# Optimization experiments

Measured on AMD Instinct MI355X. Metric: run time of the kernel, lower is better.

The kernel has to match this reference:

```python
import jax, jax.numpy as jnp
import numpy as np

B, N, C, H, D, M = 8, 4096, 512, 8, 64, 16
TOPK = 3
TAU = 0.1
DIV_REG = 0.01


def setup_inputs() -> dict:
    key = jax.random.key(0)
    ks = jax.random.split(key, 12)
    w = lambda i, shape: 0.02 * jax.random.normal(ks[i], shape, dtype=jnp.float32)
    return {
        "x": jax.random.normal(ks[0], (B, N, C), dtype=jnp.float32),
        "W_qkv": w(1, (C, 3 * C)),                    # qkv_bias=False
        "W_proj": w(2, (C, C)), "b_proj": jnp.zeros((C,), jnp.float32),
        "W_rspec": w(3, (C, H * M)), "b_rspec": jnp.zeros((H * M,), jnp.float32),
        "W_rspat": w(4, (C, H * M)), "b_rspat": jnp.zeros((H * M,), jnp.float32),
        "K_spec": w(5, (H, M, D)),                    # prototype banks (EMA buffers)
        "K_spat": w(6, (H, M, D)),
        "W_tok": w(7, (D, D)), "b_tok": jnp.zeros((D,), jnp.float32),
        "W_prot": w(8, (D, D)), "b_prot": jnp.zeros((D,), jnp.float32),
    }


def topk_mask_from_logits(logits, k):
    # keep top-k of softmax probs along last axis, renormalize
    vals = jax.lax.top_k(logits, k)[0]
    thresh = vals[..., -1:]
    mask = (logits >= thresh).astype(logits.dtype)
    probs = jax.nn.softmax(logits, axis=-1) * mask
    denom = jnp.maximum(jnp.sum(probs, axis=-1, keepdims=True), 1e-6)
    return probs / denom


def _l2norm(a, eps):
    return a / jnp.maximum(jnp.linalg.norm(a, axis=-1, keepdims=True), eps)


def reference(x, W_qkv, W_proj, b_proj, W_rspec, b_rspec, W_rspat, b_rspat,
              K_spec, K_spat, W_tok, b_tok, W_prot, b_prot):
    # qkv: [B,N,3C] -> q,k,v each [B,H,N,D]
    qkv = (x @ W_qkv).reshape(B, N, 3, H, D).transpose(2, 0, 3, 1, 4)
    q, _k, v = qkv[0], qkv[1], qkv[2]

    # routing logits [B,H,N,M] -> top-k masked probs
    r_spec = topk_mask_from_logits(
        (x @ W_rspec + b_rspec).reshape(B, N, H, M).transpose(0, 2, 1, 3), TOPK)
    r_spat = topk_mask_from_logits(
        (x @ W_rspat + b_rspat).reshape(B, N, H, M).transpose(0, 2, 1, 3), TOPK)

    # effective keys from prototype banks: [B,H,N,D]
    K_eff = (jnp.einsum('bhnm,hmd->bhnd', r_spec, K_spec)
             + jnp.einsum('bhnm,hmd->bhnd', r_spat, K_spat))
    K_norm = jax.nn.softmax(K_eff, axis=-2)          # softmax over tokens N

    # linear attention reorder: context [B,H,D,D], then Q @ context
    context = jnp.einsum('bhnd,bhne->bhde', K_norm, v)
    out = jnp.einsum('bhnd,bhde->bhne', q, context)  # note: scale unused in source
    out = out.transpose(0, 2, 1, 3).reshape(B, N, C) @ W_proj + b_proj

    # ---- contrastive aux loss ----
    t_n = _l2norm(v @ W_tok + b_tok, 1e-12)          # [B,H,N,D]
    p_spec_n = _l2norm(K_spec @ W_prot + b_prot, 1e-12)
    p_spat_n = _l2norm(K_spat @ W_prot + b_prot, 1e-12)
    sim_spec = jnp.einsum('bhnd,hmd->bhnm', t_n, p_spec_n)
    sim_spat = jnp.einsum('bhnd,hmd->bhnm', t_n, p_spat_n)
    pos_spec = jnp.sum(sim_spec * r_spec, axis=-1)
    pos_spat = jnp.sum(sim_spat * r_spat, axis=-1)
    loss_spec = -jnp.mean(pos_spec / TAU - jax.nn.logsumexp(sim_spec / TAU, axis=-1))
    loss_spat = -jnp.mean(pos_spat / TAU - jax.nn.logsumexp(sim_spat / TAU, axis=-1))
    contrastive_loss = 0.5 * (loss_spec + loss_spat)

    def diversity_loss(P):
        h, m, _d = P.shape
        p = P / jnp.maximum(jnp.linalg.norm(P, axis=-1, keepdims=True), 1e-6)
        sim = jnp.einsum('hmd,hnd->hmn', p, p)
        mask = 1.0 - jnp.eye(m, dtype=P.dtype)[None]
        return jnp.sum(sim * mask) / (h * m * (m - 1) + 1e-6)

    diversity = DIV_REG * (diversity_loss(K_spec) + diversity_loss(K_spat))
    return out, contrastive_loss, diversity
```

## Files before the change

kernel.cpp:

```cpp
#include <hip/hip_runtime.h>
#include <math.h>

#define B_ 8
#define N_ 4096
#define C_ 512
#define H_ 8
#define D_ 64
#define M_ 16
#define BN_TOK (B_*N_)
#define TAU_ 0.1f

typedef short s8v __attribute__((ext_vector_type(8)));
typedef float f4v __attribute__((ext_vector_type(4)));
typedef unsigned short u16;

__device__ __forceinline__ float wave_reduce_sum(float v){
  #pragma unroll
  for (int o = 32; o > 0; o >>= 1) v += __shfl_xor(v, o);
  return v;
}

__device__ __forceinline__ unsigned short f2b(float f){
  unsigned int u = __float_as_uint(f);
  u += 0x7fffu + ((u >> 16) & 1u);
  return (unsigned short)(u >> 16);
}

__device__ __forceinline__ float b2f(u16 b){
  return __uint_as_float(((unsigned int)b) << 16);
}

__device__ __forceinline__ s8v pack8(const float* f){
  s8v r;
  #pragma unroll
  for (int e = 0; e < 8; ++e) r[e] = (short)f2b(f[e]);
  return r;
}

__device__ __forceinline__ void gload16(const u16* g, u16* l){
  __builtin_amdgcn_global_load_lds(
      (const __attribute__((address_space(1))) unsigned int*)g,
      (__attribute__((address_space(3))) unsigned int*)l, 16, 0, 0);
}

__global__ __launch_bounds__(256) void prep_all(const float* __restrict__ x, u16* __restrict__ xb,
                                                const float* __restrict__ W_qkv,
                                                const float* __restrict__ W_rspec,
                                                const float* __restrict__ W_rspat,
                                                const float* __restrict__ W_proj,
                                                u16* __restrict__ Wt_qv,
                                                u16* __restrict__ Wt_r,
                                                u16* __restrict__ Wt_p){
  const int bid = blockIdx.x;
  if (bid < 1024) {
    const int n8 = (BN_TOK*C_)/8;
    for (int i = bid * 256 + threadIdx.x; i < n8; i += 1024*256) {
      const float4* p = (const float4*)(x + (size_t)i * 8);
      float4 a = p[0], b = p[1];
      float f[8] = {a.x,a.y,a.z,a.w,b.x,b.y,b.z,b.w};
      *(s8v*)(xb + (size_t)i * 8) = pack8(f);
    }
    return;
  }
  const int r = bid - 1024, k = threadIdx.x;
  const float* src; int ld, coff, n; u16* dst;
  if (r < 512)       { src = W_qkv;   ld = 1536; coff = 0;    n = r;        dst = Wt_qv; }
  else if (r < 1024) { src = W_qkv;   ld = 1536; coff = 1024; n = r - 512;  dst = Wt_qv + 512*512; }
  else if (r < 1152) { src = W_rspec; ld = 128;  coff = 0;    n = r - 1024; dst = Wt_r; }
  else if (r < 1280) { src = W_rspat; ld = 128;  coff = 0;    n = r - 1152; dst = Wt_r + 128*512; }
  else               { src = W_proj;  ld = 512;  coff = 0;    n = r - 1280; dst = Wt_p; }
  dst[(size_t)n*512 + k]       = f2b(src[(size_t)k*ld + coff + n]);
  dst[(size_t)n*512 + k + 256] = f2b(src[(size_t)(k+256)*ld + coff + n]);
}

template<bool OUT_BF16>
__global__ __launch_bounds__(256) void gemm_bt(const u16* __restrict__ A,
                                               const u16* __restrict__ Bt,
                                               const float* __restrict__ bias,
                                               void* __restrict__ C,
                                               int K, int lda, int ldc, int bt_bstride) {
  __shared__ __align__(16) u16 Asm[2][2][128*32];
  __shared__ __align__(16) u16 Bsm[2][2][128*32];
  const int tid = threadIdx.x;
  const int lane = tid & 63, w = tid >> 6;
  const int bm = blockIdx.x * 128, bn = blockIdx.y * 128;

  const int lrow = lane >> 2;
  const int kch  = ((lane & 3) ^ ((lane >> 3) & 3)) << 3;

  const u16* Btb = Bt + (size_t)(bm >> 12) * bt_bstride;
  const u16* Ag0 = A   + (size_t)(bm + w*16 + lrow) * lda + kch;
  const u16* Ag1 = Ag0 + (size_t)64 * lda;
  const u16* Bg0 = Btb + (size_t)(bn + w*16 + lrow) * K + kch;
  const u16* Bg1 = Bg0 + (size_t)64 * K;
  const int l0 = (w*16)*32, l1 = (w*16+64)*32;

  const int lm = lane & 15, lg = lane >> 4;
  const int w0 = (w >> 1) * 64, c0 = (w & 1) * 64;
  const int xs = (lg ^ ((lm >> 1) & 3)) << 3;

  const int NSTEP = K >> 6;

  f4v acc[4][4];
  #pragma unroll
  for (int i = 0; i < 4; ++i)
    #pragma unroll
    for (int j = 0; j < 4; ++j) acc[i][j] = (f4v){0.f,0.f,0.f,0.f};

  #define STAGE(buf, t)                                         \
    gload16(Ag0 + (t)*64,      &Asm[buf][0][l0]);               \
    gload16(Ag1 + (t)*64,      &Asm[buf][0][l1]);               \
    gload16(Ag0 + (t)*64 + 32, &Asm[buf][1][l0]);               \
    gload16(Ag1 + (t)*64 + 32, &Asm[buf][1][l1]);               \
    gload16(Bg0 + (t)*64,      &Bsm[buf][0][l0]);               \
    gload16(Bg1 + (t)*64,      &Bsm[buf][0][l1]);               \
    gload16(Bg0 + (t)*64 + 32, &Bsm[buf][1][l0]);               \
    gload16(Bg1 + (t)*64 + 32, &Bsm[buf][1][l1]);

  STAGE(0, 0)
  STAGE(1, 1)

  int cur = 0;
  for (int k = 0; k < NSTEP; ++k) {
    if (k < NSTEP - 1) asm volatile("s_waitcnt vmcnt(8)" ::: "memory");
    else               asm volatile("s_waitcnt vmcnt(0)" ::: "memory");
    __builtin_amdgcn_s_barrier();
    __builtin_amdgcn_sched_barrier(0);

    #pragma unroll
    for (int h = 0; h < 2; ++h) {
      s8v af[4], bf_[4];
      #pragma unroll
      for (int i = 0; i < 4; ++i) af[i]  = *(const s8v*)&Asm[cur][h][(w0 + 16*i + lm)*32 + xs];
      #pragma unroll
      for (int j = 0; j < 4; ++j) bf_[j] = *(const s8v*)&Bsm[cur][h][(c0 + 16*j + lm)*32 + xs];
      #pragma unroll
      for (int i = 0; i < 4; ++i)
        #pragma unroll
        for (int j = 0; j < 4; ++j)
          acc[i][j] = __builtin_amdgcn_mfma_f32_16x16x32_bf16(af[i], bf_[j], acc[i][j], 0, 0, 0);
    }

    __builtin_amdgcn_sched_barrier(0);
    __builtin_amdgcn_s_barrier();
    if (k + 2 < NSTEP) {
      STAGE(cur, k + 2)
    }
    __builtin_amdgcn_sched_barrier(0);
    cur ^= 1;
  }
  #undef STAGE

  #pragma unroll
  for (int j = 0; j < 4; ++j) {
    const int col = bn + c0 + 16*j + lm;
    const float bj = (!OUT_BF16 && bias) ? bias[col] : 0.f;
    #pragma unroll
    for (int i = 0; i < 4; ++i) {
      const int row = bm + w0 + 16*i + 4*lg;
      #pragma unroll
      for (int r = 0; r < 4; ++r) {
        if (OUT_BF16) ((u16*)C)[(size_t)(row + r) * ldc + col] = f2b(acc[i][j][r]);
        else          ((float*)C)[(size_t)(row + r) * ldc + col] = acc[i][j][r] + bj;
      }
    }
  }
}

__global__ __launch_bounds__(256) void router_topk(const float* __restrict__ logits,
                            const float* __restrict__ b_rspec, const float* __restrict__ b_rspat,
                            float* __restrict__ r_spec, float* __restrict__ r_spat,
                            u16* __restrict__ rb_spec, u16* __restrict__ rb_spat) {
  int t = blockIdx.x * blockDim.x + threadIdx.x;
  if (t >= BN_TOK * H_ * 2) return;
  int route = t & 1, h = (t >> 1) & 7, bn = t >> 4;
  int b = bn >> 12, n = bn & 4095;
  const float* lg = logits + (size_t)bn*256 + route*128 + h*16;
  const float* bias = (route ? b_rspat : b_rspec) + h*16;
  float v[16];
  #pragma unroll
  for (int m=0;m<16;++m) v[m] = lg[m] + bias[m];
  float m1=-1e30f, m2=-1e30f, m3=-1e30f;
  #pragma unroll
  for (int m=0;m<16;++m){
    float x=v[m];
    if (x>m1){m3=m2;m2=m1;m1=x;}
    else if (x>m2){m3=m2;m2=x;}
    else if (x>m3){m3=x;}
  }
  float S=0.f, Sm=0.f, e[16];
  #pragma unroll
  for (int m=0;m<16;++m){ e[m]=expf(v[m]-m1); S+=e[m]; if (v[m]>=m3) Sm+=e[m]; }
  float denom = fmaxf(Sm/S, 1e-6f);
  float inv = 1.f/(S*denom);
  size_t idx = (((size_t)b*H_ + h)*N_ + n)*16;
  float* r = (route ? r_spat : r_spec) + idx;
  u16* rb  = (route ? rb_spat : rb_spec) + idx;
  #pragma unroll
  for (int m=0;m<16;++m) {
    float val = (v[m] >= m3) ? e[m]*inv : 0.f;
    r[m] = val;
    rb[m] = f2b(val);
  }
}

__global__ __launch_bounds__(256) void context_mfma(const u16* __restrict__ rb_spec, const u16* __restrict__ rb_spat,
                               const float* __restrict__ K_spec, const float* __restrict__ K_spat,
                               const u16* __restrict__ qvb, float* __restrict__ pctx, float* __restrict__ pZ) {
  const int chunk = blockIdx.x & 15, bh = blockIdx.x >> 4;
  const int b = bh >> 3, h = bh & 7;
  const int tid = threadIdx.x;
  const int lane = tid & 63, w = tid >> 6;
  const int lm = lane & 15, lg = lane >> 4;

  __shared__ __align__(16) unsigned short Kc[64*32];
  __shared__ __align__(16) unsigned short Rs[64*32];
  __shared__ __align__(16) unsigned short Vt[64*64];
  __shared__ __align__(16) unsigned short Ps[64*64];
  __shared__ float Zs[256];

  {
    int d = tid & 63, c = tid >> 6;
    float f[8];
    #pragma unroll
    for (int u = 0; u < 8; ++u) {
      int k = c*8 + u;
      f[u] = (k < 16) ? K_spec[h*1024 + k*64 + d] : K_spat[h*1024 + (k-16)*64 + d];
    }
    *(s8v*)&Kc[d*32 + ((c ^ (d&3)) << 3)] = pack8(f);
  }

  const u16* rsg = rb_spec + ((size_t)bh*N_ + chunk*256)*16;
  const u16* rtg = rb_spat + ((size_t)bh*N_ + chunk*256)*16;
  const u16* vbase = qvb + 512 + h*64;
  const size_t tokbase = (size_t)b*N_ + chunk*256;

  f4v acc2[4];
  #pragma unroll
  for (int j = 0; j < 4; ++j) acc2[j] = (f4v){0.f,0.f,0.f,0.f};
  float zreg[4] = {0.f,0.f,0.f,0.f};

  for (int t0 = 0; t0 < 4; ++t0) {
    __syncthreads();
    {
      int n = tid & 63, c = tid >> 6;
      const u16* src = (c < 2 ? rsg : rtg) + ((size_t)(t0*64 + n))*16 + (c&1)*8;
      *(s8v*)&Rs[n*32 + ((c ^ (n&3)) << 3)] = *(const s8v*)src;
    }
    {
      int n = tid & 63, eq = tid >> 6;
      const u16* src = vbase + (tokbase + t0*64 + n)*1024 + eq*16;
      u16 f[16];
      *(s8v*)&f[0] = ((const s8v*)src)[0];
      *(s8v*)&f[8] = ((const s8v*)src)[1];
      #pragma unroll
      for (int u = 0; u < 16; ++u) {
        int e = eq*16 + u;
        Vt[e*64 + ((((n>>3) ^ (e&7)) << 3) | (n&7))] = f[u];
      }
    }
    __syncthreads();
    {
      s8v a1 = *(const s8v*)&Rs[(16*w + lm)*32 + ((lg ^ (lm&3)) << 3)];
      #pragma unroll
      for (int j = 0; j < 4; ++j) {
        s8v b1 = *(const s8v*)&Kc[(16*j + lm)*32 + ((lg ^ (lm&3)) << 3)];
        f4v c1 = (f4v){0.f,0.f,0.f,0.f};
        c1 = __builtin_amdgcn_mfma_f32_16x16x32_bf16(a1, b1, c1, 0, 0, 0);
        float p0 = expf(c1[0]), p1 = expf(c1[1]), p2 = expf(c1[2]), p3 = expf(c1[3]);
        float zz = p0 + p1 + p2 + p3;
        zz += __shfl_xor(zz, 16); zz += __shfl_xor(zz, 32);
        zreg[j] += zz;
        int d = 16*j + lm;
        int n0w = 16*w + 4*lg;
        Ps[d*64 + (((((n0w  )>>3) ^ (d&7)) << 3) | ((n0w  )&7))] = f2b(p0);
        Ps[d*64 + (((((n0w+1)>>3) ^ (d&7)) << 3) | ((n0w+1)&7))] = f2b(p1);
        Ps[d*64 + (((((n0w+2)>>3) ^ (d&7)) << 3) | ((n0w+2)&7))] = f2b(p2);
        Ps[d*64 + (((((n0w+3)>>3) ^ (d&7)) << 3) | ((n0w+3)&7))] = f2b(p3);
      }
    }
    __syncthreads();
    #pragma unroll
    for (int kb = 0; kb < 2; ++kb) {
      s8v a2 = *(const s8v*)&Vt[(16*w + lm)*64 + (((kb*4 + lg) ^ (lm&7)) << 3)];
      #pragma unroll
      for (int j = 0; j < 4; ++j) {
        s8v b2 = *(const s8v*)&Ps[(16*j + lm)*64 + (((kb*4 + lg) ^ (lm&7)) << 3)];
        acc2[j] = __builtin_amdgcn_mfma_f32_16x16x32_bf16(a2, b2, acc2[j], 0, 0, 0);
      }
    }
  }
  float* pc = pctx + (size_t)(bh*16 + chunk)*4096;
  #pragma unroll
  for (int j = 0; j < 4; ++j) {
    #pragma unroll
    for (int r = 0; r < 4; ++r)
      pc[(16*w + 4*lg + r)*64 + 16*j + lm] = acc2[j][r];
    if (lg == 0) Zs[w*64 + 16*j + lm] = zreg[j];
  }
  __syncthreads();
  if (tid < 64)
    pZ[(size_t)(bh*16 + chunk)*64 + tid] = Zs[tid] + Zs[64+tid] + Zs[128+tid] + Zs[192+tid];
}

__global__ __launch_bounds__(256) void context_reduce(const float* __restrict__ pctx, const float* __restrict__ pZ,
                              float* __restrict__ ctx) {
  const int gid = blockIdx.x * 256 + threadIdx.x;
  const int bh = gid >> 12, e = (gid >> 6) & 63, d = gid & 63;
  float z = 0.f, s = 0.f;
  for (int c = 0; c < 16; ++c) {
    z += pZ[(size_t)(bh*16 + c)*64 + d];
    s += pctx[(size_t)(bh*16 + c)*4096 + e*64 + d];
  }
  ctx[(size_t)bh*4096 + e*64 + d] = s / z;
}

__global__ __launch_bounds__(256) void cwt_kernel(const float* __restrict__ ctx, const u16* __restrict__ Wt_p,
                                                  u16* __restrict__ CWt) {
  const int bh = blockIdx.x >> 3, oct = blockIdx.x & 7;
  const int b = bh >> 3, h = bh & 7;
  const int tid = threadIdx.x;
  __shared__ float ctxS[64*64];
  __shared__ u16 WsL[64*64];
  {
    int e = tid >> 2, dq = tid & 3;
    const float4* src = (const float4*)(ctx + (size_t)bh*4096 + e*64 + dq*16);
    float4* dst = (float4*)(ctxS + e*64 + dq*16);
    dst[0] = src[0]; dst[1] = src[1]; dst[2] = src[2]; dst[3] = src[3];
  }
  const int c0 = oct * 64;
  {
    int cl = tid >> 2, eq = tid & 3;
    const s8v* src = (const s8v*)(Wt_p + (size_t)(c0 + cl)*512 + h*64 + eq*16);
    *(s8v*)&WsL[cl*64 + eq*16]     = src[0];
    *(s8v*)&WsL[cl*64 + eq*16 + 8] = src[1];
  }
  __syncthreads();
  const int d = tid & 63, cq = tid >> 6;
  for (int ci = 0; ci < 16; ++ci) {
    int cl = cq*16 + ci;
    float acc = 0.f;
    #pragma unroll
    for (int e = 0; e < 64; ++e)
      acc = fmaf(ctxS[e*64 + d], b2f(WsL[cl*64 + e]), acc);
    CWt[((size_t)b*512 + (c0 + cl))*512 + h*64 + d] = f2b(acc);
  }
}

__global__ __launch_bounds__(64) void protnorm_div(const float* __restrict__ K_spec, const float* __restrict__ K_spat,
                               const float* __restrict__ W_prot, const float* __restrict__ b_prot,
                               float* __restrict__ pnorm, float* __restrict__ pdiv) {
  const int bid = blockIdx.x;
  const int e = threadIdx.x;
  if (bid < 256) {
    int route = bid >> 7, hm = bid & 127;
    const float* Km = (route ? K_spat : K_spec) + hm*64;
    __shared__ float kv[64];
    kv[e] = Km[e];
    __syncthreads();
    float acc = b_prot[e];
    for (int dcol = 0; dcol < 64; ++dcol) acc = fmaf(kv[dcol], W_prot[dcol*64 + e], acc);
    float n2 = wave_reduce_sum(acc*acc);
    pnorm[(size_t)bid*64 + e] = acc / fmaxf(sqrtf(n2), 1e-12f);
    return;
  }
  const int db = bid - 256;
  int route = db >> 3, h = db & 7;
  const float* Km = (route ? K_spat : K_spec) + h*16*64;
  float s = 0.f, selfsum = 0.f;
  for (int m = 0; m < 16; ++m) {
    float x = Km[m*64 + e];
    float n2 = wave_reduce_sum(x*x);
    float p = x / fmaxf(sqrtf(n2), 1e-6f);
    s += p; selfsum += p*p;
  }
  float off = wave_reduce_sum(s*s - selfsum);
  if (e == 0) pdiv[db] = off;
}

__global__ __launch_bounds__(256) void contrastive_mfma(const u16* __restrict__ qvb,
                                   const float* __restrict__ r_spec, const float* __restrict__ r_spat,
                                   const float* __restrict__ W_tok, const float* __restrict__ b_tok,
                                   const float* __restrict__ pnorm, float* __restrict__ pcontr) {
  const int tile = blockIdx.x & 255;
  const int h = blockIdx.x >> 8;
  const int t0 = tile * 128;
  const int b = t0 >> 12;
  const int n0 = t0 & 4095;
  const int tid = threadIdx.x;
  const int lane = tid & 63, w = tid >> 6;
  const int lm = lane & 15, lg = lane >> 4;

  __shared__ __align__(16) unsigned short Usm[128*72];
  __shared__ __align__(16) unsigned short Wsm[64*72];
  __shared__ __align__(16) unsigned short Psm[32*72];
  __shared__ float nrmS[128];
  __shared__ float btkS[64];
  __shared__ float bred[2][4];
  float* Uf = (float*)Usm;

  {
    const int vr = tid >> 1, vh = tid & 1;
    const u16* vg = qvb + (size_t)(b*N_ + n0 + vr)*1024 + 512 + h*64 + vh*32;
    #pragma unroll
    for (int c = 0; c < 4; ++c) *(s8v*)&Usm[vr*72 + vh*32 + c*8] = ((const s8v*)vg)[c];
  }
  {
    const int e = tid & 63, kh = tid >> 6;
    float f[16];
    #pragma unroll
    for (int rr = 0; rr < 16; ++rr) f[rr] = W_tok[(size_t)(kh*16+rr)*64 + e];
    *(s8v*)&Wsm[e*72 + kh*16]     = pack8(&f[0]);
    *(s8v*)&Wsm[e*72 + kh*16 + 8] = pack8(&f[8]);
  }
  if (tid < 128) {
    const int proto = tid >> 2, q4 = tid & 3;
    const int src = (proto < 16) ? (h*16 + proto) : (128 + h*16 + (proto-16));
    const float* pg = pnorm + (size_t)src*64 + q4*16;
    float f[16];
    #pragma unroll
    for (int i = 0; i < 4; ++i) {
      float4 v4 = ((const float4*)pg)[i];
      f[4*i]=v4.x; f[4*i+1]=v4.y; f[4*i+2]=v4.z; f[4*i+3]=v4.w;
    }
    *(s8v*)&Psm[proto*72 + q4*16]     = pack8(&f[0]);
    *(s8v*)&Psm[proto*72 + q4*16 + 8] = pack8(&f[8]);
  }
  if (tid < 64) btkS[tid] = b_tok[tid];
  __syncthreads();

  f4v acc[2][4];
  #pragma unroll
  for (int i=0;i<2;++i)
    #pragma unroll
    for (int j=0;j<4;++j) acc[i][j] = (f4v){0.f,0.f,0.f,0.f};
  {
    s8v bf0[4], bf1[4];
    #pragma unroll
    for (int j=0;j<4;++j) {
      bf0[j] = *(const s8v*)&Wsm[(j*16+lm)*72 + lg*8];
      bf1[j] = *(const s8v*)&Wsm[(j*16+lm)*72 + 32 + lg*8];
    }
    #pragma unroll
    for (int i=0;i<2;++i) {
      s8v af0 = *(const s8v*)&Usm[(w*32+16*i+lm)*72 + lg*8];
      s8v af1 = *(const s8v*)&Usm[(w*32+16*i+lm)*72 + 32 + lg*8];
      #pragma unroll
      for (int j=0;j<4;++j) {
        acc[i][j] = __builtin_amdgcn_mfma_f32_16x16x32_bf16(af0, bf0[j], acc[i][j], 0, 0, 0);
        acc[i][j] = __builtin_amdgcn_mfma_f32_16x16x32_bf16(af1, bf1[j], acc[i][j], 0, 0, 0);
      }
    }
  }
  #pragma unroll
  for (int i=0;i<2;++i) {
    #pragma unroll
    for (int r=0;r<4;++r) {
      float s = 0.f;
      #pragma unroll
      for (int j=0;j<4;++j) {
        float val = acc[i][j][r] + btkS[j*16+lm];
        acc[i][j][r] = val;
        s += val*val;
      }
      s += __shfl_xor(s,1); s += __shfl_xor(s,2); s += __shfl_xor(s,4); s += __shfl_xor(s,8);
      if (lm == 0) nrmS[w*32 + 16*i + lg*4 + r] = s;
    }
  }
  #pragma unroll
  for (int i=0;i<2;++i)
    #pragma unroll
    for (int j=0;j<4;++j)
      #pragma unroll
      for (int r=0;r<4;++r)
        Usm[(w*32+16*i+lg*4+r)*72 + j*16+lm] = f2b(acc[i][j][r]);
  __syncthreads();

  f4v acc2[2][2];
  #pragma unroll
  for (int i=0;i<2;++i)
    #pragma unroll
    for (int j=0;j<2;++j) acc2[i][j] = (f4v){0.f,0.f,0.f,0.f};
  {
    s8v bf0[2], bf1[2];
    #pragma unroll
    for (int j=0;j<2;++j) {
      bf0[j] = *(const s8v*)&Psm[(j*16+lm)*72 + lg*8];
      bf1[j] = *(const s8v*)&Psm[(j*16+lm)*72 + 32 + lg*8];
    }
    #pragma unroll
    for (int i=0;i<2;++i) {
      s8v af0 = *(const s8v*)&Usm[(w*32+16*i+lm)*72 + lg*8];
      s8v af1 = *(const s8v*)&Usm[(w*32+16*i+lm)*72 + 32 + lg*8];
      #pragma unroll
      for (int j=0;j<2;++j) {
        acc2[i][j] = __builtin_amdgcn_mfma_f32_16x16x32_bf16(af0, bf0[j], acc2[i][j], 0, 0, 0);
        acc2[i][j] = __builtin_amdgcn_mfma_f32_16x16x32_bf16(af1, bf1[j], acc2[i][j], 0, 0, 0);
      }
    }
  }
  #pragma unroll
  for (int i=0;i<2;++i)
    #pragma unroll
    for (int j=0;j<2;++j)
      #pragma unroll
      for (int r=0;r<4;++r)
        Uf[(w*32+16*i+lg*4+r)*36 + j*16+lm] = acc2[i][j][r];
  __syncthreads();

  float l = 0.f;
  {
    const int tt = tid >> 1, route = tid & 1;
    float inv = 1.f / fmaxf(sqrtf(nrmS[tt]), 1e-12f);
    const float* rg = (route ? r_spat : r_spec) + (((size_t)b*H_ + h)*N_ + n0 + tt)*16;
    float s0[16];
    #pragma unroll
    for (int m=0;m<16;++m) s0[m] = Uf[tt*36 + route*16 + m]*inv;
    float pos = 0.f, mx = -1e30f;
    #pragma unroll
    for (int m=0;m<16;++m) {
      pos += s0[m]*rg[m];
      mx = fmaxf(mx, s0[m]);
    }
    float z = 0.f;
    #pragma unroll
    for (int m=0;m<16;++m) z += expf((s0[m]-mx)/TAU_);
    l = pos/TAU_ - (mx/TAU_ + logf(z));
  }
  float lspec = (tid & 1) ? 0.f : l;
  float lspat = (tid & 1) ? l : 0.f;
  lspec = wave_reduce_sum(lspec);
  lspat = wave_reduce_sum(lspat);
  if (lane == 0) { bred[0][w]=lspec; bred[1][w]=lspat; }
  __syncthreads();
  if (tid == 0) {
    pcontr[2*blockIdx.x]     = bred[0][0]+bred[0][1]+bred[0][2]+bred[0][3];
    pcontr[2*blockIdx.x + 1] = bred[1][0]+bred[1][1]+bred[1][2]+bred[1][3];
  }
}

__global__ __launch_bounds__(256) void finalize_kernel(const float* __restrict__ pcontr,
                                                       const float* __restrict__ pdiv,
                                                       float* __restrict__ tail) {
  __shared__ float red[2][4];
  const int tid = threadIdx.x, lane = tid & 63, w = tid >> 6;
  float ls = 0.f, lt = 0.f;
  for (int k = tid; k < 2048; k += 256) { ls += pcontr[2*k]; lt += pcontr[2*k + 1]; }
  ls = wave_reduce_sum(ls);
  lt = wave_reduce_sum(lt);
  if (lane == 0) { red[0][w] = ls; red[1][w] = lt; }
  __syncthreads();
  if (tid == 0) {
    float sspec = red[0][0]+red[0][1]+red[0][2]+red[0][3];
    float sspat = red[1][0]+red[1][1]+red[1][2]+red[1][3];
    float dspec = 0.f, dspat = 0.f;
    for (int k = 0; k < 8; ++k) { dspec += pdiv[k]; dspat += pdiv[8+k]; }
    float loss_spec = -(sspec / (float)(B_*H_*N_));
    float loss_spat = -(sspat / (float)(B_*H_*N_));
    float denom = (float)(H_*M_*(M_-1)) + 1e-6f;
    tail[0] = 0.5f*(loss_spec + loss_spat);
    tail[1] = 0.01f * (dspec/denom + dspat/denom);
  }
}

extern "C" void kernel_launch(void* const* d_in, const int* in_sizes, int n_in,
                              void* d_out, int out_size, void* d_ws, size_t ws_size,
                              hipStream_t stream) {
  const float* x       = (const float*)d_in[0];
  const float* W_qkv   = (const float*)d_in[1];
  const float* W_proj  = (const float*)d_in[2];
  const float* b_proj  = (const float*)d_in[3];
  const float* W_rspec = (const float*)d_in[4];
  const float* b_rspec = (const float*)d_in[5];
  const float* W_rspat = (const float*)d_in[6];
  const float* b_rspat = (const float*)d_in[7];
  const float* K_spec  = (const float*)d_in[8];
  const float* K_spat  = (const float*)d_in[9];
  const float* W_tok   = (const float*)d_in[10];
  const float* b_tok   = (const float*)d_in[11];
  const float* W_prot  = (const float*)d_in[12];
  const float* b_prot  = (const float*)d_in[13];
  float* out = (float*)d_out;

  float* ws = (float*)d_ws;
  u16*   qvb     = (u16*)ws;
  float* logits  = ws + 16777216;
  float* pctx    = ws + 16777216;
  float* pZ      = ws + 16777216 + 4194304;
  float* r_spec  = ws + 25165824;
  float* r_spat  = ws + 29360128;
  u16*   rb_spec = (u16*)(ws + 33554432);
  u16*   rb_spat = (u16*)(ws + 35651584);
  u16*   xb      = (u16*)(ws + 37748736);
  u16*   Wt_qv   = (u16*)(ws + 46137344);
  u16*   Wt_r    = (u16*)(ws + 46399488);
  u16*   Wt_p    = (u16*)(ws + 46465024);
  float* ctxb    = ws + 46596096;
  float* pnorm   = ws + 46858240;
  float* pcontr  = ws + 46874624;
  float* pdiv    = ws + 46878720;
  u16*   CWt     = (u16*)(ws + 46878736);

  dim3 blk256(256);

  prep_all<<<2816, blk256, 0, stream>>>(x, xb, W_qkv, W_rspec, W_rspat, W_proj, Wt_qv, Wt_r, Wt_p);

  gemm_bt<false><<<dim3(256,2), blk256, 0, stream>>>(xb, Wt_r, nullptr, logits, 512, 512, 256, 0);
  router_topk<<<2048, blk256, 0, stream>>>(logits, b_rspec, b_rspat, r_spec, r_spat, rb_spec, rb_spat);
  gemm_bt<true><<<dim3(256,8), blk256, 0, stream>>>(xb, Wt_qv, nullptr, qvb, 512, 512, 1024, 0);
  context_mfma<<<1024, blk256, 0, stream>>>(rb_spec, rb_spat, K_spec, K_spat, qvb, pctx, pZ);
  context_reduce<<<1024, blk256, 0, stream>>>(pctx, pZ, ctxb);
  cwt_kernel<<<512, blk256, 0, stream>>>(ctxb, Wt_p, CWt);
  protnorm_div<<<272, dim3(64), 0, stream>>>(K_spec, K_spat, W_prot, b_prot, pnorm, pdiv);
  contrastive_mfma<<<2048, blk256, 0, stream>>>(qvb, r_spec, r_spat, W_tok, b_tok, pnorm, pcontr);
  gemm_bt<false><<<dim3(256,4), blk256, 0, stream>>>(qvb, CWt, b_proj, out, 512, 1024, 512, 512*512);
  finalize_kernel<<<1, blk256, 0, stream>>>(pcontr, pdiv, out + 16777216);
}
```

Baseline: 334.1 us.

## Fuse router and QV GEMMs into one launch with XCD-aware tile mapping

Runs the routing-logit GEMM and the Q/V projection GEMM as a single launch over the contiguous concatenated transposed weights. Column tiles below the split are written as bf16 to qvb, and the rest go as fp32 to logits. Block IDs are also remapped so that each XCD owns a contiguous range of row tiles, which keeps shared A tiles in that XCD's L2. The aim is to cut one launch, fill the GPU better, and improve cache reuse. The cost is extra template and epilogue branching, and the fusion relies on Wt_r sitting directly after Wt_qv in the workspace.

```diff
diff --git a/kernel.cpp b/kernel.cpp
--- a/kernel.cpp
+++ b/kernel.cpp
@@ -73,17 +73,24 @@
   dst[(size_t)n*512 + k + 256] = f2b(src[(size_t)(k+256)*ld + coff + n]);
 }
 
-template<bool OUT_BF16>
+template<int MODE>
 __global__ __launch_bounds__(256) void gemm_bt(const u16* __restrict__ A,
                                                const u16* __restrict__ Bt,
                                                const float* __restrict__ bias,
                                                void* __restrict__ C,
-                                               int K, int lda, int ldc, int bt_bstride) {
+                                               float* __restrict__ C2,
+                                               int K, int lda, int ldc, int ldc2,
+                                               int split, int bt_bstride, int nm) {
   __shared__ __align__(16) u16 Asm[2][2][128*32];
   __shared__ __align__(16) u16 Bsm[2][2][128*32];
   const int tid = threadIdx.x;
   const int lane = tid & 63, w = tid >> 6;
-  const int bm = blockIdx.x * 128, bn = blockIdx.y * 128;
+
+  const int bid = blockIdx.x;
+  const int xcd = bid & 7, j = bid >> 3;
+  const int nmx = nm >> 3;
+  const int bm = (xcd * nmx + (j % nmx)) * 128;
+  const int bn = (j / nmx) * 128;
 
   const int lrow = lane >> 2;
   const int kch  = ((lane & 3) ^ ((lane >> 3) & 3)) << 3;
@@ -105,7 +112,7 @@
   #pragma unroll
   for (int i = 0; i < 4; ++i)
     #pragma unroll
-    for (int j = 0; j < 4; ++j) acc[i][j] = (f4v){0.f,0.f,0.f,0.f};
+    for (int j2 = 0; j2 < 4; ++j2) acc[i][j2] = (f4v){0.f,0.f,0.f,0.f};
 
   #define STAGE(buf, t)                                         \
     gload16(Ag0 + (t)*64,      &Asm[buf][0][l0]);               \
@@ -133,12 +140,12 @@
       #pragma unroll
       for (int i = 0; i < 4; ++i) af[i]  = *(const s8v*)&Asm[cur][h][(w0 + 16*i + lm)*32 + xs];
       #pragma unroll
-      for (int j = 0; j < 4; ++j) bf_[j] = *(const s8v*)&Bsm[cur][h][(c0 + 16*j + lm)*32 + xs];
+      for (int j2 = 0; j2 < 4; ++j2) bf_[j2] = *(const s8v*)&Bsm[cur][h][(c0 + 16*j2 + lm)*32 + xs];
       #pragma unroll
       for (int i = 0; i < 4; ++i)
         #pragma unroll
-        for (int j = 0; j < 4; ++j)
-          acc[i][j] = __builtin_amdgcn_mfma_f32_16x16x32_bf16(af[i], bf_[j], acc[i][j], 0, 0, 0);
+        for (int j2 = 0; j2 < 4; ++j2)
+          acc[i][j2] = __builtin_amdgcn_mfma_f32_16x16x32_bf16(af[i], bf_[j2], acc[i][j2], 0, 0, 0);
     }
 
     __builtin_amdgcn_sched_barrier(0);
@@ -151,17 +158,19 @@
   }
   #undef STAGE
 
-  #pragma unroll
-  for (int j = 0; j < 4; ++j) {
-    const int col = bn + c0 + 16*j + lm;
-    const float bj = (!OUT_BF16 && bias) ? bias[col] : 0.f;
+  const bool tobf = (MODE == 1) || (MODE == 2 && bn < split);
+  #pragma unroll
+  for (int j2 = 0; j2 < 4; ++j2) {
+    const int col = bn + c0 + 16*j2 + lm;
+    const float bj = (MODE == 0 && bias) ? bias[col] : 0.f;
     #pragma unroll
     for (int i = 0; i < 4; ++i) {
       const int row = bm + w0 + 16*i + 4*lg;
       #pragma unroll
       for (int r = 0; r < 4; ++r) {
-        if (OUT_BF16) ((u16*)C)[(size_t)(row + r) * ldc + col] = f2b(acc[i][j][r]);
-        else          ((float*)C)[(size_t)(row + r) * ldc + col] = acc[i][j][r] + bj;
+        if (tobf)            ((u16*)C)[(size_t)(row + r) * ldc + col] = f2b(acc[i][j2][r]);
+        else if (MODE == 2)  C2[(size_t)(row + r) * ldc2 + (col - split)] = acc[i][j2][r];
+        else                 ((float*)C)[(size_t)(row + r) * ldc + col] = acc[i][j2][r] + bj;
       }
     }
   }
@@ -605,14 +614,15 @@
 
   prep_all<<<2816, blk256, 0, stream>>>(x, xb, W_qkv, W_rspec, W_rspat, W_proj, Wt_qv, Wt_r, Wt_p);
 
-  gemm_bt<false><<<dim3(256,2), blk256, 0, stream>>>(xb, Wt_r, nullptr, logits, 512, 512, 256, 0);
+  gemm_bt<2><<<2560, blk256, 0, stream>>>(xb, Wt_qv, nullptr, qvb, logits,
+                                          512, 512, 1024, 256, 1024, 0, 256);
   router_topk<<<2048, blk256, 0, stream>>>(logits, b_rspec, b_rspat, r_spec, r_spat, rb_spec, rb_spat);
-  gemm_bt<true><<<dim3(256,8), blk256, 0, stream>>>(xb, Wt_qv, nullptr, qvb, 512, 512, 1024, 0);
   context_mfma<<<1024, blk256, 0, stream>>>(rb_spec, rb_spat, K_spec, K_spat, qvb, pctx, pZ);
   context_reduce<<<1024, blk256, 0, stream>>>(pctx, pZ, ctxb);
   cwt_kernel<<<512, blk256, 0, stream>>>(ctxb, Wt_p, CWt);
   protnorm_div<<<272, dim3(64), 0, stream>>>(K_spec, K_spat, W_prot, b_prot, pnorm, pdiv);
   contrastive_mfma<<<2048, blk256, 0, stream>>>(qvb, r_spec, r_spat, W_tok, b_tok, pnorm, pcontr);
-  gemm_bt<false><<<dim3(256,4), blk256, 0, stream>>>(qvb, CWt, b_proj, out, 512, 1024, 512, 512*512);
+  gemm_bt<0><<<1024, blk256, 0, stream>>>(qvb, CWt, b_proj, out, nullptr,
+                                          512, 1024, 512, 0, 1 << 30, 512*512, 256);
   finalize_kernel<<<1, blk256, 0, stream>>>(pcontr, pdiv, out + 16777216);
 }
```

Result: no change. 339.1 us (+1.5%).

## Fold Q projection into per-batch output weights, skip materializing Q

Applied to the files above, without the earlier changes.

Instead of computing Q = x·Wq and then Q·(ctx·Wproj), the code precomputes per-batch combined weights W2 = Wq·(ctx·Wproj) with a small GEMM and applies them directly to x. The QV GEMM shrinks to a V-only GEMM, so Q is no longer written to memory and read back, and the final GEMM uses K=512 over x instead of reading Q. It adds a small extra GEMM per batch and one more bf16 rounding step on the combined weights, which changes numerics slightly.

```diff
diff --git a/kernel.cpp b/kernel.cpp
--- a/kernel.cpp
+++ b/kernel.cpp
@@ -48,13 +48,15 @@
                                                 const float* __restrict__ W_rspec,
                                                 const float* __restrict__ W_rspat,
                                                 const float* __restrict__ W_proj,
-                                                u16* __restrict__ Wt_qv,
+                                                u16* __restrict__ Wqk,
+                                                u16* __restrict__ Wt_v,
                                                 u16* __restrict__ Wt_r,
                                                 u16* __restrict__ Wt_p){
   const int bid = blockIdx.x;
+  const int t = threadIdx.x;
   if (bid < 1024) {
     const int n8 = (BN_TOK*C_)/8;
-    for (int i = bid * 256 + threadIdx.x; i < n8; i += 1024*256) {
+    for (int i = bid * 256 + t; i < n8; i += 1024*256) {
       const float4* p = (const float4*)(x + (size_t)i * 8);
       float4 a = p[0], b = p[1];
       float f[8] = {a.x,a.y,a.z,a.w,b.x,b.y,b.z,b.w};
@@ -62,18 +64,23 @@
     }
     return;
   }
-  const int r = bid - 1024, k = threadIdx.x;
+  if (bid < 1536) {
+    const int k = bid - 1024;
+    Wqk[(size_t)k*512 + t]       = f2b(W_qkv[(size_t)k*1536 + t]);
+    Wqk[(size_t)k*512 + t + 256] = f2b(W_qkv[(size_t)k*1536 + t + 256]);
+    return;
+  }
+  const int r = bid - 1536;
   const float* src; int ld, coff, n; u16* dst;
-  if (r < 512)       { src = W_qkv;   ld = 1536; coff = 0;    n = r;        dst = Wt_qv; }
-  else if (r < 1024) { src = W_qkv;   ld = 1536; coff = 1024; n = r - 512;  dst = Wt_qv + 512*512; }
-  else if (r < 1152) { src = W_rspec; ld = 128;  coff = 0;    n = r - 1024; dst = Wt_r; }
-  else if (r < 1280) { src = W_rspat; ld = 128;  coff = 0;    n = r - 1152; dst = Wt_r + 128*512; }
-  else               { src = W_proj;  ld = 512;  coff = 0;    n = r - 1280; dst = Wt_p; }
-  dst[(size_t)n*512 + k]       = f2b(src[(size_t)k*ld + coff + n]);
-  dst[(size_t)n*512 + k + 256] = f2b(src[(size_t)(k+256)*ld + coff + n]);
-}
-
-template<bool OUT_BF16>
+  if (r < 512)       { src = W_qkv;   ld = 1536; coff = 1024; n = r;        dst = Wt_v; }
+  else if (r < 640)  { src = W_rspec; ld = 128;  coff = 0;    n = r - 512;  dst = Wt_r; }
+  else if (r < 768)  { src = W_rspat; ld = 128;  coff = 0;    n = r - 640;  dst = Wt_r + 128*512; }
+  else               { src = W_proj;  ld = 512;  coff = 0;    n = r - 768;  dst = Wt_p; }
+  dst[(size_t)n*512 + t]       = f2b(src[(size_t)t*ld + coff + n]);
+  dst[(size_t)n*512 + t + 256] = f2b(src[(size_t)(t+256)*ld + coff + n]);
+}
+
+template<int MODE>
 __global__ __launch_bounds__(256) void gemm_bt(const u16* __restrict__ A,
                                                const u16* __restrict__ Bt,
                                                const float* __restrict__ bias,
@@ -107,15 +114,15 @@
     #pragma unroll
     for (int j = 0; j < 4; ++j) acc[i][j] = (f4v){0.f,0.f,0.f,0.f};
 
-  #define STAGE(buf, t)                                         \
-    gload16(Ag0 + (t)*64,      &Asm[buf][0][l0]);               \
-    gload16(Ag1 + (t)*64,      &Asm[buf][0][l1]);               \
-    gload16(Ag0 + (t)*64 + 32, &Asm[buf][1][l0]);               \
-    gload16(Ag1 + (t)*64 + 32, &Asm[buf][1][l1]);               \
-    gload16(Bg0 + (t)*64,      &Bsm[buf][0][l0]);               \
-    gload16(Bg1 + (t)*64,      &Bsm[buf][0][l1]);               \
-    gload16(Bg0 + (t)*64 + 32, &Bsm[buf][1][l0]);               \
-    gload16(Bg1 + (t)*64 + 32, &Bsm[buf][1][l1]);
+  #define STAGE(buf, tt)                                        \
+    gload16(Ag0 + (tt)*64,      &Asm[buf][0][l0]);              \
+    gload16(Ag1 + (tt)*64,      &Asm[buf][0][l1]);              \
+    gload16(Ag0 + (tt)*64 + 32, &Asm[buf][1][l0]);              \
+    gload16(Ag1 + (tt)*64 + 32, &Asm[buf][1][l1]);              \
+    gload16(Bg0 + (tt)*64,      &Bsm[buf][0][l0]);              \
+    gload16(Bg1 + (tt)*64,      &Bsm[buf][0][l1]);              \
+    gload16(Bg0 + (tt)*64 + 32, &Bsm[buf][1][l0]);              \
+    gload16(Bg1 + (tt)*64 + 32, &Bsm[buf][1][l1]);
 
   STAGE(0, 0)
   STAGE(1, 1)
@@ -154,14 +161,14 @@
   #pragma unroll
   for (int j = 0; j < 4; ++j) {
     const int col = bn + c0 + 16*j + lm;
-    const float bj = (!OUT_BF16 && bias) ? bias[col] : 0.f;
+    const float bj = (MODE == 0 && bias) ? bias[col] : 0.f;
     #pragma unroll
     for (int i = 0; i < 4; ++i) {
       const int row = bm + w0 + 16*i + 4*lg;
       #pragma unroll
       for (int r = 0; r < 4; ++r) {
-        if (OUT_BF16) ((u16*)C)[(size_t)(row + r) * ldc + col] = f2b(acc[i][j][r]);
-        else          ((float*)C)[(size_t)(row + r) * ldc + col] = acc[i][j][r] + bj;
+        if (MODE == 1) ((u16*)C)[(size_t)(row + r) * ldc + col] = f2b(acc[i][j][r]);
+        else           ((float*)C)[(size_t)(row + r) * ldc + col] = acc[i][j][r] + bj;
       }
     }
   }
@@ -206,7 +213,7 @@
 
 __global__ __launch_bounds__(256) void context_mfma(const u16* __restrict__ rb_spec, const u16* __restrict__ rb_spat,
                                const float* __restrict__ K_spec, const float* __restrict__ K_spat,
-                               const u16* __restrict__ qvb, float* __restrict__ pctx, float* __restrict__ pZ) {
+                               const u16* __restrict__ vb, float* __restrict__ pctx, float* __restrict__ pZ) {
   const int chunk = blockIdx.x & 15, bh = blockIdx.x >> 4;
   const int b = bh >> 3, h = bh & 7;
   const int tid = threadIdx.x;
@@ -232,7 +239,7 @@
 
   const u16* rsg = rb_spec + ((size_t)bh*N_ + chunk*256)*16;
   const u16* rtg = rb_spat + ((size_t)bh*N_ + chunk*256)*16;
-  const u16* vbase = qvb + 512 + h*64;
+  const u16* vbase = vb + h*64;
   const size_t tokbase = (size_t)b*N_ + chunk*256;
 
   f4v acc2[4];
@@ -249,7 +256,7 @@
     }
     {
       int n = tid & 63, eq = tid >> 6;
-      const u16* src = vbase + (tokbase + t0*64 + n)*1024 + eq*16;
+      const u16* src = vbase + (tokbase + t0*64 + n)*512 + eq*16;
       u16 f[16];
       *(s8v*)&f[0] = ((const s8v*)src)[0];
       *(s8v*)&f[8] = ((const s8v*)src)[1];
@@ -378,7 +385,7 @@
   if (e == 0) pdiv[db] = off;
 }
 
-__global__ __launch_bounds__(256) void contrastive_mfma(const u16* __restrict__ qvb,
+__global__ __launch_bounds__(256) void contrastive_mfma(const u16* __restrict__ vb,
                                    const float* __restrict__ r_spec, const float* __restrict__ r_spat,
                                    const float* __restrict__ W_tok, const float* __restrict__ b_tok,
                                    const float* __restrict__ pnorm, float* __restrict__ pcontr) {
@@ -401,7 +408,7 @@
 
   {
     const int vr = tid >> 1, vh = tid & 1;
-    const u16* vg = qvb + (size_t)(b*N_ + n0 + vr)*1024 + 512 + h*64 + vh*32;
+    const u16* vg = vb + (size_t)(b*N_ + n0 + vr)*512 + h*64 + vh*32;
     #pragma unroll
     for (int c = 0; c < 4; ++c) *(s8v*)&Usm[vr*72 + vh*32 + c*8] = ((const s8v*)vg)[c];
   }
@@ -583,36 +590,39 @@
   float* out = (float*)d_out;
 
   float* ws = (float*)d_ws;
-  u16*   qvb     = (u16*)ws;
-  float* logits  = ws + 16777216;
-  float* pctx    = ws + 16777216;
-  float* pZ      = ws + 16777216 + 4194304;
-  float* r_spec  = ws + 25165824;
-  float* r_spat  = ws + 29360128;
-  u16*   rb_spec = (u16*)(ws + 33554432);
-  u16*   rb_spat = (u16*)(ws + 35651584);
-  u16*   xb      = (u16*)(ws + 37748736);
-  u16*   Wt_qv   = (u16*)(ws + 46137344);
-  u16*   Wt_r    = (u16*)(ws + 46399488);
-  u16*   Wt_p    = (u16*)(ws + 46465024);
-  float* ctxb    = ws + 46596096;
-  float* pnorm   = ws + 46858240;
-  float* pcontr  = ws + 46874624;
-  float* pdiv    = ws + 46878720;
-  u16*   CWt     = (u16*)(ws + 46878736);
+  u16*   vb      = (u16*)ws;
+  float* logits  = ws + 8388608;
+  float* pctx    = ws + 8388608;
+  float* pZ      = ws + 8388608 + 4194304;
+  float* r_spec  = ws + 16777216;
+  float* r_spat  = ws + 20971520;
+  u16*   rb_spec = (u16*)(ws + 25165824);
+  u16*   rb_spat = (u16*)(ws + 27262976);
+  u16*   xb      = (u16*)(ws + 29360128);
+  u16*   Wqk     = (u16*)(ws + 37748736);
+  u16*   Wt_v    = (u16*)(ws + 37879808);
+  u16*   Wt_r    = (u16*)(ws + 38010880);
+  u16*   Wt_p    = (u16*)(ws + 38076416);
+  float* ctxb    = ws + 38207488;
+  float* pnorm   = ws + 38469632;
+  float* pcontr  = ws + 38486016;
+  float* pdiv    = ws + 38490112;
+  u16*   CWt     = (u16*)(ws + 38490128);
+  u16*   W2t     = (u16*)(ws + 39538704);
 
   dim3 blk256(256);
 
-  prep_all<<<2816, blk256, 0, stream>>>(x, xb, W_qkv, W_rspec, W_rspat, W_proj, Wt_qv, Wt_r, Wt_p);
-
-  gemm_bt<false><<<dim3(256,2), blk256, 0, stream>>>(xb, Wt_r, nullptr, logits, 512, 512, 256, 0);
+  prep_all<<<2816, blk256, 0, stream>>>(x, xb, W_qkv, W_rspec, W_rspat, W_proj, Wqk, Wt_v, Wt_r, Wt_p);
+
+  gemm_bt<0><<<dim3(256,2), blk256, 0, stream>>>(xb, Wt_r, nullptr, logits, 512, 512, 256, 0);
   router_topk<<<2048, blk256, 0, stream>>>(logits, b_rspec, b_rspat, r_spec, r_spat, rb_spec, rb_spat);
-  gemm_bt<true><<<dim3(256,8), blk256, 0, stream>>>(xb, Wt_qv, nullptr, qvb, 512, 512, 1024, 0);
-  context_mfma<<<1024, blk256, 0, stream>>>(rb_spec, rb_spat, K_spec, K_spat, qvb, pctx, pZ);
+  gemm_bt<1><<<dim3(256,4), blk256, 0, stream>>>(xb, Wt_v, nullptr, vb, 512, 512, 512, 0);
+  context_mfma<<<1024, blk256, 0, stream>>>(rb_spec, rb_spat, K_spec, K_spat, vb, pctx, pZ);
   context_reduce<<<1024, blk256, 0, stream>>>(pctx, pZ, ctxb);
   cwt_kernel<<<512, blk256, 0, stream>>>(ctxb, Wt_p, CWt);
+  gemm_bt<1><<<dim3(32,4), blk256, 0, stream>>>(CWt, Wqk, nullptr, W2t, 512, 512, 512, 0);
   protnorm_div<<<272, dim3(64), 0, stream>>>(K_spec, K_spat, W_prot, b_prot, pnorm, pdiv);
-  contrastive_mfma<<<2048, blk256, 0, stream>>>(qvb, r_spec, r_spat, W_tok, b_tok, pnorm, pcontr);
-  gemm_bt<false><<<dim3(256,4), blk256, 0, stream>>>(qvb, CWt, b_proj, out, 512, 1024, 512, 512*512);
+  contrastive_mfma<<<2048, blk256, 0, stream>>>(vb, r_spec, r_spat, W_tok, b_tok, pnorm, pcontr);
+  gemm_bt<0><<<dim3(256,4), blk256, 0, stream>>>(xb, W2t, b_proj, out, 512, 512, 512, 512*512);
   finalize_kernel<<<1, blk256, 0, stream>>>(pcontr, pdiv, out + 16777216);
 }
```

Result: faster. 323.0 us (-3.3%).
